# Optimization experiments

Hardware: AMD Instinct MI355X
Metric: run time of the kernel (lower is better)

## Reference

```python
import jax, jax.numpy as jnp
import numpy as np

N, S, H, FA = 16, 64, 256, 256  # batch, sentences, memory_size, fact_attn_hidden


def setup_inputs() -> dict:
    key = jax.random.key(0)
    ks = jax.random.split(key, 12)
    g = lambda k, shp: (jax.random.normal(k, shp, jnp.float32) * 0.05)
    return dict(
        facts=jax.random.normal(ks[0], (N, S, H), jnp.float32),
        prevM=jax.random.normal(ks[1], (N, S, H), jnp.float32),
        questions=jax.random.normal(ks[2], (N, S, H), jnp.float32),
        doc_len=jax.random.randint(ks[3], (N,), S // 2, S + 1),
        z1_w=g(ks[4], (FA, 4 * H)), z1_b=jnp.zeros((FA,), jnp.float32),
        z2_w=g(ks[5], (1, FA)), z2_b=jnp.zeros((1,), jnp.float32),
        Wr_w=g(ks[6], (H, H)), Wr_b=jnp.zeros((H,), jnp.float32),
        Ur_w=g(ks[7], (H, H)), Ur_b=jnp.zeros((H,), jnp.float32),
        W_w=g(ks[8], (H, H)), W_b=jnp.zeros((H,), jnp.float32),
        U_w=g(ks[9], (H, H)), U_b=jnp.zeros((H,), jnp.float32),
        nm_w=g(ks[10], (H, 3 * H)), nm_b=jnp.zeros((H,), jnp.float32),
    )


def reference(facts, prevM, questions, doc_len,
              z1_w, z1_b, z2_w, z2_b,
              Wr_w, Wr_b, Ur_w, Ur_b, W_w, W_b, U_w, U_b,
              nm_w, nm_b):
    n, s, h = facts.shape
    # ---- make_interaction: pairwise features (query axis = dim1, fact/key axis = dim2)
    f = facts[:, None, :, :]       # (N,1,S,H) broadcast over queries
    m = prevM[:, :, None, :]       # (N,S,1,H) broadcast over keys
    q = questions[:, :, None, :]   # (N,S,1,H)
    z = jnp.concatenate([f * q, f * m, jnp.abs(f - q), jnp.abs(f - m)], axis=-1)  # (N,S,S,4H)
    Gh = jnp.tanh(z @ z1_w.T + z1_b)               # (N,S,S,FA)
    G = (Gh @ z2_w.T + z2_b)[..., 0]               # (N,S,S)
    mask = (jnp.arange(s) < doc_len[:, None]).astype(G.dtype)  # (N,S) key mask
    Gm = G * mask[:, None, :]
    Gm = jnp.where(Gm == 0, -jnp.inf, Gm)          # faithful to G[G==0] = -inf
    attn = jax.nn.softmax(Gm, axis=2)              # (N,S,S)

    # ---- AttentionalGRU over the S facts for each of the N*S query rows
    B = n * s
    fb = jnp.broadcast_to(facts[:, None], (n, s, s, h)).reshape(B, s, h)  # (B,S,H)
    gb = attn.reshape(B, s)                                               # (B,S)

    def step(C, xs):
        fact, gt = xs                                   # fact: (B,H), gt: (B,)
        r = jax.nn.sigmoid(fact @ Wr_w.T + Wr_b + C @ Ur_w.T + Ur_b)
        h_t = jnp.tanh(fact @ W_w.T + W_b + r * (C @ U_w.T + U_b))
        gt = gt[:, None]
        return gt * h_t + (1.0 - gt) * C, None

    C0 = jnp.zeros((B, h), facts.dtype)
    C, _ = jax.lax.scan(step, C0, (fb.transpose(1, 0, 2), gb.T))  # scan over S steps
    C = C.reshape(n, s, h)

    # ---- memory update (dropouts are identity in eval mode)
    concat = jnp.concatenate([prevM, C, questions], axis=-1)  # (N,S,3H)
    next_mem = jax.nn.relu(concat @ nm_w.T + nm_b)            # (N,S,H)
    return next_mem, attn
```

## Files before the change

### kernel.cpp

```cpp
#include <hip/hip_runtime.h>
#include <hip/hip_bf16.h>
#include <math.h>

#define NB 16
#define SS 64
#define HH 256
#define FAA 256

using short8 = __attribute__((ext_vector_type(8))) short;
using f32x4  = __attribute__((ext_vector_type(4))) float;

__device__ __forceinline__ unsigned short f2bf(float f) {
  union { float f; unsigned int u; } x; x.f = f;
  unsigned int u = x.u;
  return (unsigned short)((u + 0x7FFFu + ((u >> 16) & 1u)) >> 16);
}
__device__ __forceinline__ unsigned int cvtpk(float a, float b) {
  unsigned int r;
  asm("v_cvt_pk_bf16_f32 %0, %1, %2" : "=v"(r) : "v"(a), "v"(b));
  return r;
}
__device__ __forceinline__ float sel4(const f32x4 a, int q) {
  const float s01 = (q & 1) ? a[1] : a[0];
  const float s23 = (q & 1) ? a[3] : a[2];
  return (q & 2) ? s23 : s01;
}

__global__ void prolog_cvt(const float* __restrict__ z1w, const float* __restrict__ Ur,
                           const float* __restrict__ U, const float* __restrict__ nmw,
                           const float* __restrict__ pm, const float* __restrict__ qs,
                           unsigned short* __restrict__ z1wbf, unsigned short* __restrict__ wcatbf,
                           unsigned short* __restrict__ nmbf, unsigned short* __restrict__ pmbf,
                           unsigned short* __restrict__ qbf) {
  int idx = blockIdx.x * 256 + threadIdx.x;
  if (idx < 262144) { z1wbf[idx] = f2bf(z1w[idx]); return; }
  idx -= 262144;
  if (idx < 131072) {
    int o = idx >> 8, s = idx & 255;
    int t = s & 31;
    int cc = (s & ~31) + (t >> 1) + ((t & 1) << 4);
    wcatbf[idx] = f2bf(o < 256 ? Ur[o * 256 + cc] : U[(o - 256) * 256 + cc]);
    return;
  }
  idx -= 131072;
  if (idx < 196608) {
    int o = idx / 768, k = idx - o * 768;
    int kk = k;
    if (k >= 256 && k < 512) {
      int s = k - 256, t = s & 31;
      kk = 256 + (s & ~31) + (t >> 1) + ((t & 1) << 4);
    }
    nmbf[idx] = f2bf(nmw[o * 768 + kk]);
    return;
  }
  idx -= 196608;
  if (idx < 262144) { pmbf[idx] = f2bf(pm[idx]); return; }
  idx -= 262144;
  if (idx < 262144) { qbf[idx] = f2bf(qs[idx]); return; }
}

__global__ __launch_bounds__(256) void fact_proj(
    const float* __restrict__ facts, const float* __restrict__ Wr, const float* __restrict__ Wrb,
    const float* __restrict__ Urb, const float* __restrict__ Ww, const float* __restrict__ Wb,
    float* __restrict__ FWr, float* __restrict__ FW) {
  __shared__ float fl[4][HH];
  const int b0 = blockIdx.x * 4;
  const int tid = threadIdx.x;
#pragma unroll
  for (int r = 0; r < 4; ++r) fl[r][tid] = facts[(b0 + r) * HH + tid];
  __syncthreads();
  float ar[4] = {0.f, 0.f, 0.f, 0.f}, aw[4] = {0.f, 0.f, 0.f, 0.f};
  const float4* wr = (const float4*)(Wr + tid * HH);
  const float4* ww = (const float4*)(Ww + tid * HH);
  for (int d4 = 0; d4 < 64; ++d4) {
    float4 a = wr[d4], b = ww[d4];
#pragma unroll
    for (int r = 0; r < 4; ++r) {
      float4 f = *(const float4*)&fl[r][d4 * 4];
      ar[r] += a.x * f.x + a.y * f.y + a.z * f.z + a.w * f.w;
      aw[r] += b.x * f.x + b.y * f.y + b.z * f.z + b.w * f.w;
    }
  }
  const float br = Wrb[tid] + Urb[tid], bw = Wb[tid];
#pragma unroll
  for (int r = 0; r < 4; ++r) {
    FWr[(b0 + r) * HH + tid] = ar[r] + br;
    FW[(b0 + r) * HH + tid] = aw[r] + bw;
  }
}

__global__ __launch_bounds__(512, 4) void gate_gemm(
    const float* __restrict__ facts, const float* __restrict__ prevM,
    const float* __restrict__ questions, const unsigned short* __restrict__ z1wbf,
    const float* __restrict__ z1b, const float* __restrict__ z2w,
    const float* __restrict__ z2b, const int* __restrict__ doc_len,
    float* __restrict__ attn) {
  __shared__ unsigned short Ab[2][128 * 32];
  __shared__ unsigned short Bb[2][256 * 32];
  __shared__ float Gpart[128][4];

  const int bi = blockIdx.x;
  const int n = bi >> 5, i0 = (bi & 31) * 2;
  const int tid = threadIdx.x;
  const int w = tid >> 6, l = tid & 63;
  const int rg = w >> 2, cg = w & 3;
  const int l15 = l & 15, q = l >> 4;
  const int t15 = tid & 15, jb = tid >> 4;

  const float* fn = facts + n * SS * HH;
  const float* qn = questions + (n * SS + i0) * HH;
  const float* mn = prevM + (n * SS + i0) * HH;

  auto stageB = [&](int buf, int hc, int s) {
    const int kb = s * 256 + hc * 32;
    const int swz = ((l & 3) ^ ((l >> 2) & 3)) * 8;
#pragma unroll
    for (int j = 0; j < 2; ++j) {
      const int colg = w * 32 + j * 16 + (l >> 2);
      const unsigned short* src = z1wbf + colg * 1024 + kb + swz;
      __builtin_amdgcn_global_load_lds(src, Bb[buf] + (w * 32 + j * 16) * 32, 16, 0, 0);
    }
  };

  auto buildA = [&](int buf, int s, float2 f0, float2 f1, float2 q0, float2 q1,
                    float2 m0, float2 m1) {
    unsigned int* dst = (unsigned int*)Ab[buf];
    const int dsw = t15 ^ ((jb & 3) << 2);
    const float2 o0 = (s & 1) ? m0 : q0;
    const float2 o1 = (s & 1) ? m1 : q1;
#pragma unroll
    for (int pl = 0; pl < 2; ++pl) {
      const float fx = pl ? f1.x : f0.x;
      const float fy = pl ? f1.y : f0.y;
#pragma unroll
      for (int il = 0; il < 2; ++il) {
        const int row = il * 64 + pl * 32 + jb;
        const float ox = il ? o1.x : o0.x;
        const float oy = il ? o1.y : o0.y;
        float a, b;
        if (s < 2) { a = fx * ox;         b = fy * oy; }
        else       { a = fabsf(fx - ox);  b = fabsf(fy - oy); }
        dst[row * 16 + dsw] = cvtpk(a, b);
      }
    }
  };

  const f32x4 zero4 = {0.f, 0.f, 0.f, 0.f};
  f32x4 acc[4][4];
#pragma unroll
  for (int a = 0; a < 4; ++a)
#pragma unroll
    for (int b = 0; b < 4; ++b) acc[a][b] = zero4;

  auto mfmaStep = [&](int buf) {
    short8 Bfr[4];
#pragma unroll
    for (int nf = 0; nf < 4; ++nf) {
      const int col = cg * 64 + nf * 16 + l15;
      Bfr[nf] = *(const short8*)&Bb[buf][col * 32 + (q ^ (l15 & 3)) * 8];
    }
    __builtin_amdgcn_s_setprio(1);
#pragma unroll
    for (int mf = 0; mf < 4; ++mf) {
      const int row = rg * 64 + mf * 16 + l15;
      const short8 Afm = *(const short8*)&Ab[buf][row * 32 + (q ^ (l15 & 3)) * 8];
#pragma unroll
      for (int nf = 0; nf < 4; ++nf)
        acc[mf][nf] = __builtin_amdgcn_mfma_f32_16x16x32_bf16(Afm, Bfr[nf], acc[mf][nf], 0, 0, 0);
    }
    __builtin_amdgcn_s_setprio(0);
  };

  const int hh2 = t15 * 2;
  auto pf = [&](int hc, float2& f0, float2& f1, float2& q0, float2& q1,
                float2& m0, float2& m1) {
    const int h = hc * 32 + hh2;
    f0 = *(const float2*)(fn + jb * HH + h);
    f1 = *(const float2*)(fn + (jb + 32) * HH + h);
    q0 = *(const float2*)(qn + h);
    q1 = *(const float2*)(qn + HH + h);
    m0 = *(const float2*)(mn + h);
    m1 = *(const float2*)(mn + HH + h);
  };

  float2 Rf0, Rf1, Rq0, Rq1, Rm0, Rm1;
  float2 Sf0, Sf1, Sq0, Sq1, Sm0, Sm1;
  pf(0, Rf0, Rf1, Rq0, Rq1, Rm0, Rm1);
  stageB(0, 0, 0);
  buildA(0, 0, Rf0, Rf1, Rq0, Rq1, Rm0, Rm1);
  __syncthreads();

  int buf = 0;
  for (int hc = 0; hc < 8; ++hc) {
    stageB(buf ^ 1, hc, 1);
    buildA(buf ^ 1, 1, Rf0, Rf1, Rq0, Rq1, Rm0, Rm1);
    mfmaStep(buf);
    __syncthreads();
    buf ^= 1;
    stageB(buf ^ 1, hc, 2);
    buildA(buf ^ 1, 2, Rf0, Rf1, Rq0, Rq1, Rm0, Rm1);
    mfmaStep(buf);
    __syncthreads();
    buf ^= 1;
    stageB(buf ^ 1, hc, 3);
    buildA(buf ^ 1, 3, Rf0, Rf1, Rq0, Rq1, Rm0, Rm1);
    if (hc < 7) pf(hc + 1, Sf0, Sf1, Sq0, Sq1, Sm0, Sm1);
    mfmaStep(buf);
    __syncthreads();
    buf ^= 1;
    if (hc < 7) {
      stageB(buf ^ 1, hc + 1, 0);
      buildA(buf ^ 1, 0, Sf0, Sf1, Sq0, Sq1, Sm0, Sm1);
    }
    mfmaStep(buf);
    __syncthreads();
    buf ^= 1;
    Rf0 = Sf0; Rf1 = Sf1; Rq0 = Sq0; Rq1 = Sq1; Rm0 = Sm0; Rm1 = Sm1;
  }

  float psum[4][4];
#pragma unroll
  for (int mf = 0; mf < 4; ++mf)
#pragma unroll
    for (int v = 0; v < 4; ++v) psum[mf][v] = 0.f;

#pragma unroll
  for (int nf = 0; nf < 4; ++nf) {
    const int k = cg * 64 + nf * 16 + l15;
    const float zb = z1b[k], zw = z2w[k];
#pragma unroll
    for (int mf = 0; mf < 4; ++mf)
#pragma unroll
      for (int v = 0; v < 4; ++v) {
        const float x = acc[mf][nf][v] + zb;
        const float e = __expf(2.f * x);
        const float t = 1.f - 2.f / (e + 1.f);
        psum[mf][v] += zw * t;
      }
  }
#pragma unroll
  for (int d = 1; d < 16; d <<= 1)
#pragma unroll
    for (int mf = 0; mf < 4; ++mf)
#pragma unroll
      for (int v = 0; v < 4; ++v) psum[mf][v] += __shfl_xor(psum[mf][v], d, 64);
  if (l15 == 0) {
#pragma unroll
    for (int mf = 0; mf < 4; ++mf)
#pragma unroll
      for (int v = 0; v < 4; ++v)
        Gpart[rg * 64 + mf * 16 + q * 4 + v][cg] = psum[mf][v];
  }
  __syncthreads();
  if (tid < 128) {
    const float gg = Gpart[tid][0] + Gpart[tid][1] + Gpart[tid][2] + Gpart[tid][3] + z2b[0];
    const int i = i0 + (tid >> 6), j = tid & 63;
    const int dl = doc_len[n];
    const float x = (j < dl && gg != 0.0f) ? gg : -INFINITY;
    float mx = x;
#pragma unroll
    for (int d = 1; d < 64; d <<= 1) mx = fmaxf(mx, __shfl_xor(mx, d, 64));
    const float e = (x == -INFINITY) ? 0.f : __expf(x - mx);
    float s = e;
#pragma unroll
    for (int d = 1; d < 64; d <<= 1) s += __shfl_xor(s, d, 64);
    attn[(n * SS + i) * SS + j] = e / s;
  }
}

__global__ __launch_bounds__(512, 2) void gru_scan(
    const unsigned short* __restrict__ wcat, const float* __restrict__ FWr,
    const float* __restrict__ FW, const float* __restrict__ Ub,
    const float* __restrict__ attn, unsigned short* __restrict__ Cout) {
  __shared__ unsigned short Cbf[2][4 * 272];
  __shared__ float attn_sT[64 * 4];

  const int bi = blockIdx.x, n = bi >> 4, i0 = (bi & 15) * 4;
  const int tid = threadIdx.x, w = tid >> 6, l = tid & 63;
  const int l15 = l & 15, q = l >> 4;
  const int h0 = w * 32 + l15;

  short8 Bf[8][4];
#pragma unroll
  for (int f = 0; f < 4; ++f) {
    const int wrow = ((f >> 1) ? 256 : 0) + w * 32 + (f & 1) * 16 + l15;
    const unsigned short* bb = wcat + wrow * 256 + q * 8;
#pragma unroll
    for (int kt = 0; kt < 8; ++kt)
      Bf[kt][f] = *(const short8*)(bb + kt * 32);
  }

  const float ub0 = Ub[h0], ub1 = Ub[h0 + 16];

  for (int e = tid; e < 64 * 4; e += 512)
    attn_sT[e] = attn[(n * SS + i0 + (e & 3)) * SS + (e >> 2)];
  for (int e = tid; e < 544; e += 512)
    ((unsigned int*)Cbf[0])[e] = 0u;
  __syncthreads();

  const float* fwr_g = FWr + n * SS * HH;
  const float* fw_g  = FW + n * SS * HH;

  float cm0 = 0.f, cm1 = 0.f;
  float fr0 = fwr_g[h0], fr1 = fwr_g[h0 + 16];
  float fc0 = fw_g[h0],  fc1 = fw_g[h0 + 16];

  for (int t = 0; t < 64; ++t) {
    const int cur = t & 1;
    const unsigned short* Cr = Cbf[cur];
    unsigned int* Cw = (unsigned int*)Cbf[cur ^ 1];

    short8 Af[8];
    const int arow = (l15 & 3) * 272;
#pragma unroll
    for (int kt = 0; kt < 8; ++kt)
      Af[kt] = *(const short8*)&Cr[arow + kt * 32 + q * 8];

    float nr0 = 0.f, nr1 = 0.f, nc0 = 0.f, nc1 = 0.f;
    if (t < 63) {
      nr0 = fwr_g[(t + 1) * HH + h0];
      nr1 = fwr_g[(t + 1) * HH + h0 + 16];
      nc0 = fw_g[(t + 1) * HH + h0];
      nc1 = fw_g[(t + 1) * HH + h0 + 16];
    }

    const f32x4 z4 = {0.f, 0.f, 0.f, 0.f};
    f32x4 acc[4];
#pragma unroll
    for (int f = 0; f < 4; ++f) acc[f] = z4;
    __builtin_amdgcn_s_setprio(1);
#pragma unroll
    for (int kt = 0; kt < 8; ++kt)
#pragma unroll
      for (int f = 0; f < 4; ++f)
        acc[f] = __builtin_amdgcn_mfma_f32_16x16x32_bf16(Af[kt], Bf[kt][f], acc[f], 0, 0, 0);
    __builtin_amdgcn_s_setprio(0);

    const float yr0 = sel4(acc[0], q), yr1 = sel4(acc[1], q);
    const float yu0 = sel4(acc[2], q), yu1 = sel4(acc[3], q);
    const float g = attn_sT[t * 4 + q];

    const float r0 = 1.f / (1.f + __expf(-(fr0 + yr0)));
    const float x0 = fc0 + r0 * (yu0 + ub0);
    const float e0 = __expf(2.f * x0);
    const float h0t = 1.f - 2.f / (e0 + 1.f);
    cm0 += g * (h0t - cm0);

    const float r1 = 1.f / (1.f + __expf(-(fr1 + yr1)));
    const float x1 = fc1 + r1 * (yu1 + ub1);
    const float e1 = __expf(2.f * x1);
    const float h1t = 1.f - 2.f / (e1 + 1.f);
    cm1 += g * (h1t - cm1);

    Cw[q * 136 + w * 16 + l15] = cvtpk(cm0, cm1);

    fr0 = nr0; fr1 = nr1; fc0 = nc0; fc1 = nc1;
    __syncthreads();
  }

  {
    const int row = tid >> 7, wo = tid & 127;
    ((unsigned int*)Cout)[(n * SS + i0 + row) * 128 + wo] =
        *(const unsigned int*)&Cbf[0][row * 272 + wo * 2];
  }
}

__global__ __launch_bounds__(256) void next_mem_gemm(
    const unsigned short* __restrict__ pmbf, const unsigned short* __restrict__ cbf,
    const unsigned short* __restrict__ qbf, const unsigned short* __restrict__ nmbf,
    const float* __restrict__ nmb, float* __restrict__ out) {
  __shared__ unsigned short A[64][40];
  const int bi = blockIdx.x;
  const int rb = bi >> 3, cb = bi & 7;
  const int r0 = rb * 64, c0 = cb * 32;
  const int tid = threadIdx.x, w = tid >> 6, l = tid & 63;
  const int l15 = l & 15, q = l >> 4;

  f32x4 acc[2];
  const f32x4 z4 = {0.f, 0.f, 0.f, 0.f};
#pragma unroll
  for (int nf = 0; nf < 2; ++nf) acc[nf] = z4;

  for (int kt = 0; kt < 24; ++kt) {
    const int kg = kt * 32;
    const unsigned short* src =
        kg < 256 ? (pmbf + kg) : (kg < 512 ? (cbf + kg - 256) : (qbf + kg - 512));
    const int kk = (tid & 15) * 2;
#pragma unroll
    for (int ps = 0; ps < 4; ++ps) {
      const int row = ps * 16 + (tid >> 4);
      *(unsigned int*)&A[row][kk] = *(const unsigned int*)(src + (r0 + row) * HH + kk);
    }
    __syncthreads();
    short8 Bfr[2];
#pragma unroll
    for (int nf = 0; nf < 2; ++nf)
      Bfr[nf] = *(const short8*)(nmbf + (c0 + nf * 16 + l15) * 768 + kg + q * 8);
    const short8 Af = *(const short8*)&A[w * 16 + l15][q * 8];
#pragma unroll
    for (int nf = 0; nf < 2; ++nf)
      acc[nf] = __builtin_amdgcn_mfma_f32_16x16x32_bf16(Af, Bfr[nf], acc[nf], 0, 0, 0);
    __syncthreads();
  }
#pragma unroll
  for (int nf = 0; nf < 2; ++nf) {
    const int col = c0 + nf * 16 + l15;
    const float bv = nmb[col];
#pragma unroll
    for (int v = 0; v < 4; ++v) {
      const int grow = r0 + w * 16 + q * 4 + v;
      out[grow * HH + col] = fmaxf(acc[nf][v] + bv, 0.f);
    }
  }
}

extern "C" void kernel_launch(void* const* d_in, const int* in_sizes, int n_in,
                              void* d_out, int out_size, void* d_ws, size_t ws_size,
                              hipStream_t stream) {
  const float* facts     = (const float*)d_in[0];
  const float* prevM     = (const float*)d_in[1];
  const float* questions = (const float*)d_in[2];
  const int*   doc_len   = (const int*)d_in[3];
  const float* z1w = (const float*)d_in[4];
  const float* z1b = (const float*)d_in[5];
  const float* z2w = (const float*)d_in[6];
  const float* z2b = (const float*)d_in[7];
  const float* Wrw = (const float*)d_in[8];
  const float* Wrb = (const float*)d_in[9];
  const float* Urw = (const float*)d_in[10];
  const float* Urb = (const float*)d_in[11];
  const float* Ww  = (const float*)d_in[12];
  const float* Wb  = (const float*)d_in[13];
  const float* Uw  = (const float*)d_in[14];
  const float* Ub  = (const float*)d_in[15];
  const float* nmw = (const float*)d_in[16];
  const float* nmb = (const float*)d_in[17];

  char* ws = (char*)d_ws;
  unsigned short* z1wbf  = (unsigned short*)(ws + 0);
  unsigned short* wcatbf = (unsigned short*)(ws + 524288);
  unsigned short* nmbf   = (unsigned short*)(ws + 786432);
  unsigned short* pmbf   = (unsigned short*)(ws + 1179648);
  unsigned short* qbf    = (unsigned short*)(ws + 1703936);
  float* FWr = (float*)(ws + 2490368);
  float* FW  = (float*)(ws + 3538944);
  unsigned short* cbf = (unsigned short*)(ws + 4587520);

  float* out  = (float*)d_out;
  float* attn = out + NB * SS * HH;

  prolog_cvt<<<4352, 256, 0, stream>>>(z1w, Urw, Uw, nmw, prevM, questions,
                                       z1wbf, wcatbf, nmbf, pmbf, qbf);
  fact_proj<<<256, 256, 0, stream>>>(facts, Wrw, Wrb, Urb, Ww, Wb, FWr, FW);
  gate_gemm<<<512, 512, 0, stream>>>(facts, prevM, questions, z1wbf, z1b, z2w, z2b,
                                     doc_len, attn);
  gru_scan<<<256, 512, 0, stream>>>(wcatbf, FWr, FW, Ub, attn, cbf);
  next_mem_gemm<<<128, 256, 0, stream>>>(pmbf, cbf, qbf, nmbf, nmb, out);
}
```

Measured before the change: 244.8 us.

## Fuse prologue kernels, pad GRU LDS, deepen prefetch, split MFMA chains

Merges the bf16 conversion prologue and the fact projection into one launch, with extra blocks taking the projection path. In the GRU scan it adds a large unused LDS array to limit occupancy to one block per CU, prefetches the fact projections two steps ahead instead of one, splits the MFMA accumulation into two interleaved chains, and swaps __syncthreads for an inline waitcnt plus barrier. These aim to cut launch overhead, global-load latency and per-step dependency stalls in the serial scan. The padding gives up occupancy, and the hand-written barrier relies on lgkmcnt alone to cover the LDS writes.

Measured after the change: 287.4 us. 1.17x slower.

```diff
diff --git a/kernel.cpp b/kernel.cpp
--- a/kernel.cpp
+++ b/kernel.cpp
@@ -26,12 +26,44 @@
   return (q & 2) ? s23 : s01;
 }
 
-__global__ void prolog_cvt(const float* __restrict__ z1w, const float* __restrict__ Ur,
-                           const float* __restrict__ U, const float* __restrict__ nmw,
-                           const float* __restrict__ pm, const float* __restrict__ qs,
-                           unsigned short* __restrict__ z1wbf, unsigned short* __restrict__ wcatbf,
-                           unsigned short* __restrict__ nmbf, unsigned short* __restrict__ pmbf,
-                           unsigned short* __restrict__ qbf) {
+__global__ __launch_bounds__(256) void prolog_fused(
+    const float* __restrict__ z1w, const float* __restrict__ Ur,
+    const float* __restrict__ U, const float* __restrict__ nmw,
+    const float* __restrict__ pm, const float* __restrict__ qs,
+    unsigned short* __restrict__ z1wbf, unsigned short* __restrict__ wcatbf,
+    unsigned short* __restrict__ nmbf, unsigned short* __restrict__ pmbf,
+    unsigned short* __restrict__ qbf,
+    const float* __restrict__ facts, const float* __restrict__ Wr,
+    const float* __restrict__ Wrb, const float* __restrict__ Urb,
+    const float* __restrict__ Ww, const float* __restrict__ Wb,
+    float* __restrict__ FWr, float* __restrict__ FW) {
+  __shared__ float fl[4][HH];
+  if (blockIdx.x >= 4352) {
+    const int b0 = (blockIdx.x - 4352) * 4;
+    const int tid = threadIdx.x;
+#pragma unroll
+    for (int r = 0; r < 4; ++r) fl[r][tid] = facts[(b0 + r) * HH + tid];
+    __syncthreads();
+    float ar[4] = {0.f, 0.f, 0.f, 0.f}, aw[4] = {0.f, 0.f, 0.f, 0.f};
+    const float4* wr = (const float4*)(Wr + tid * HH);
+    const float4* ww = (const float4*)(Ww + tid * HH);
+    for (int d4 = 0; d4 < 64; ++d4) {
+      float4 a = wr[d4], b = ww[d4];
+#pragma unroll
+      for (int r = 0; r < 4; ++r) {
+        float4 f = *(const float4*)&fl[r][d4 * 4];
+        ar[r] += a.x * f.x + a.y * f.y + a.z * f.z + a.w * f.w;
+        aw[r] += b.x * f.x + b.y * f.y + b.z * f.z + b.w * f.w;
+      }
+    }
+    const float br = Wrb[tid] + Urb[tid], bw = Wb[tid];
+#pragma unroll
+    for (int r = 0; r < 4; ++r) {
+      FWr[(b0 + r) * HH + tid] = ar[r] + br;
+      FW[(b0 + r) * HH + tid] = aw[r] + bw;
+    }
+    return;
+  }
   int idx = blockIdx.x * 256 + threadIdx.x;
   if (idx < 262144) { z1wbf[idx] = f2bf(z1w[idx]); return; }
   idx -= 262144;
@@ -57,36 +89,6 @@
   if (idx < 262144) { pmbf[idx] = f2bf(pm[idx]); return; }
   idx -= 262144;
   if (idx < 262144) { qbf[idx] = f2bf(qs[idx]); return; }
-}
-
-__global__ __launch_bounds__(256) void fact_proj(
-    const float* __restrict__ facts, const float* __restrict__ Wr, const float* __restrict__ Wrb,
-    const float* __restrict__ Urb, const float* __restrict__ Ww, const float* __restrict__ Wb,
-    float* __restrict__ FWr, float* __restrict__ FW) {
-  __shared__ float fl[4][HH];
-  const int b0 = blockIdx.x * 4;
-  const int tid = threadIdx.x;
-#pragma unroll
-  for (int r = 0; r < 4; ++r) fl[r][tid] = facts[(b0 + r) * HH + tid];
-  __syncthreads();
-  float ar[4] = {0.f, 0.f, 0.f, 0.f}, aw[4] = {0.f, 0.f, 0.f, 0.f};
-  const float4* wr = (const float4*)(Wr + tid * HH);
-  const float4* ww = (const float4*)(Ww + tid * HH);
-  for (int d4 = 0; d4 < 64; ++d4) {
-    float4 a = wr[d4], b = ww[d4];
-#pragma unroll
-    for (int r = 0; r < 4; ++r) {
-      float4 f = *(const float4*)&fl[r][d4 * 4];
-      ar[r] += a.x * f.x + a.y * f.y + a.z * f.z + a.w * f.w;
-      aw[r] += b.x * f.x + b.y * f.y + b.z * f.z + b.w * f.w;
-    }
-  }
-  const float br = Wrb[tid] + Urb[tid], bw = Wb[tid];
-#pragma unroll
-  for (int r = 0; r < 4; ++r) {
-    FWr[(b0 + r) * HH + tid] = ar[r] + br;
-    FW[(b0 + r) * HH + tid] = aw[r] + bw;
-  }
 }
 
 __global__ __launch_bounds__(512, 4) void gate_gemm(
@@ -274,11 +276,14 @@
     const float* __restrict__ attn, unsigned short* __restrict__ Cout) {
   __shared__ unsigned short Cbf[2][4 * 272];
   __shared__ float attn_sT[64 * 4];
+  __shared__ float lds_pad[20608];
 
   const int bi = blockIdx.x, n = bi >> 4, i0 = (bi & 15) * 4;
   const int tid = threadIdx.x, w = tid >> 6, l = tid & 63;
   const int l15 = l & 15, q = l >> 4;
   const int h0 = w * 32 + l15;
+
+  if (tid == 0) lds_pad[0] = 0.f;
 
   short8 Bf[8][4];
 #pragma unroll
@@ -302,8 +307,10 @@
   const float* fw_g  = FW + n * SS * HH;
 
   float cm0 = 0.f, cm1 = 0.f;
-  float fr0 = fwr_g[h0], fr1 = fwr_g[h0 + 16];
-  float fc0 = fw_g[h0],  fc1 = fw_g[h0 + 16];
+  float frA0 = fwr_g[h0], frA1 = fwr_g[h0 + 16];
+  float fcA0 = fw_g[h0],  fcA1 = fw_g[h0 + 16];
+  float frB0 = fwr_g[HH + h0], frB1 = fwr_g[HH + h0 + 16];
+  float fcB0 = fw_g[HH + h0],  fcB1 = fw_g[HH + h0 + 16];
 
   for (int t = 0; t < 64; ++t) {
     const int cur = t & 1;
@@ -317,45 +324,50 @@
       Af[kt] = *(const short8*)&Cr[arow + kt * 32 + q * 8];
 
     float nr0 = 0.f, nr1 = 0.f, nc0 = 0.f, nc1 = 0.f;
-    if (t < 63) {
-      nr0 = fwr_g[(t + 1) * HH + h0];
-      nr1 = fwr_g[(t + 1) * HH + h0 + 16];
-      nc0 = fw_g[(t + 1) * HH + h0];
-      nc1 = fw_g[(t + 1) * HH + h0 + 16];
+    if (t < 62) {
+      const float* a = fwr_g + (t + 2) * HH;
+      const float* b = fw_g + (t + 2) * HH;
+      nr0 = a[h0]; nr1 = a[h0 + 16];
+      nc0 = b[h0]; nc1 = b[h0 + 16];
     }
 
     const f32x4 z4 = {0.f, 0.f, 0.f, 0.f};
-    f32x4 acc[4];
-#pragma unroll
-    for (int f = 0; f < 4; ++f) acc[f] = z4;
+    f32x4 a0 = z4, a1 = z4, a2 = z4, a3 = z4;
     __builtin_amdgcn_s_setprio(1);
 #pragma unroll
-    for (int kt = 0; kt < 8; ++kt)
-#pragma unroll
-      for (int f = 0; f < 4; ++f)
-        acc[f] = __builtin_amdgcn_mfma_f32_16x16x32_bf16(Af[kt], Bf[kt][f], acc[f], 0, 0, 0);
+    for (int kt = 0; kt < 8; ++kt) {
+      a0 = __builtin_amdgcn_mfma_f32_16x16x32_bf16(Af[kt], Bf[kt][0], a0, 0, 0, 0);
+      a2 = __builtin_amdgcn_mfma_f32_16x16x32_bf16(Af[kt], Bf[kt][2], a2, 0, 0, 0);
+    }
+#pragma unroll
+    for (int kt = 0; kt < 8; ++kt) {
+      a1 = __builtin_amdgcn_mfma_f32_16x16x32_bf16(Af[kt], Bf[kt][1], a1, 0, 0, 0);
+      a3 = __builtin_amdgcn_mfma_f32_16x16x32_bf16(Af[kt], Bf[kt][3], a3, 0, 0, 0);
+    }
     __builtin_amdgcn_s_setprio(0);
 
-    const float yr0 = sel4(acc[0], q), yr1 = sel4(acc[1], q);
-    const float yu0 = sel4(acc[2], q), yu1 = sel4(acc[3], q);
     const float g = attn_sT[t * 4 + q];
 
-    const float r0 = 1.f / (1.f + __expf(-(fr0 + yr0)));
-    const float x0 = fc0 + r0 * (yu0 + ub0);
+    const float yr0 = sel4(a0, q), yu0 = sel4(a2, q);
+    const float r0 = 1.f / (1.f + __expf(-(frA0 + yr0)));
+    const float x0 = fcA0 + r0 * (yu0 + ub0);
     const float e0 = __expf(2.f * x0);
     const float h0t = 1.f - 2.f / (e0 + 1.f);
     cm0 += g * (h0t - cm0);
 
-    const float r1 = 1.f / (1.f + __expf(-(fr1 + yr1)));
-    const float x1 = fc1 + r1 * (yu1 + ub1);
+    const float yr1 = sel4(a1, q), yu1 = sel4(a3, q);
+    const float r1 = 1.f / (1.f + __expf(-(frA1 + yr1)));
+    const float x1 = fcA1 + r1 * (yu1 + ub1);
     const float e1 = __expf(2.f * x1);
     const float h1t = 1.f - 2.f / (e1 + 1.f);
     cm1 += g * (h1t - cm1);
 
     Cw[q * 136 + w * 16 + l15] = cvtpk(cm0, cm1);
 
-    fr0 = nr0; fr1 = nr1; fc0 = nc0; fc1 = nc1;
-    __syncthreads();
+    frA0 = frB0; frA1 = frB1; fcA0 = fcB0; fcA1 = fcB1;
+    frB0 = nr0; frB1 = nr1; fcB0 = nc0; fcB1 = nc1;
+
+    asm volatile("s_waitcnt lgkmcnt(0)\n\ts_barrier" ::: "memory");
   }
 
   {
@@ -449,9 +461,9 @@
   float* out  = (float*)d_out;
   float* attn = out + NB * SS * HH;
 
-  prolog_cvt<<<4352, 256, 0, stream>>>(z1w, Urw, Uw, nmw, prevM, questions,
-                                       z1wbf, wcatbf, nmbf, pmbf, qbf);
-  fact_proj<<<256, 256, 0, stream>>>(facts, Wrw, Wrb, Urb, Ww, Wb, FWr, FW);
+  prolog_fused<<<4608, 256, 0, stream>>>(z1w, Urw, Uw, nmw, prevM, questions,
+                                         z1wbf, wcatbf, nmbf, pmbf, qbf,
+                                         facts, Wrw, Wrb, Urb, Ww, Wb, FWr, FW);
   gate_gemm<<<512, 512, 0, stream>>>(facts, prevM, questions, z1wbf, z1b, z2w, z2b,
                                      doc_len, attn);
   gru_scan<<<256, 512, 0, stream>>>(wcatbf, FWr, FW, Ub, attn, cbf);
```
